# Performance work log

Hardware: AMD Instinct MI355X
Metric: run time of the kernel (lower is better)

Reference implementation:

```python
import jax, jax.numpy as jnp
import numpy as np

B, S, D, H = 4, 2048, 1024, 16
HD = D // H  # head dim = 64


def setup_inputs() -> dict:
    key = jax.random.key(0)
    ks = jax.random.split(key, 12)
    s = 1.0 / np.sqrt(D)
    return {
        "query": jax.random.normal(ks[0], (B, S, D), jnp.float32),
        "key": jax.random.normal(ks[1], (B, S, D), jnp.float32),
        "value": jax.random.normal(ks[2], (B, S, D), jnp.float32),
        "attention_mask": jnp.zeros((B, S, S), jnp.float32),
        "Wq": jax.random.normal(ks[3], (D, D), jnp.float32) * s,
        "bq": jax.random.normal(ks[4], (D,), jnp.float32) * s,
        "Wk": jax.random.normal(ks[5], (D, D), jnp.float32) * s,
        "bk": jax.random.normal(ks[6], (D,), jnp.float32) * s,
        "Wv": jax.random.normal(ks[7], (D, D), jnp.float32) * s,
        "bv": jax.random.normal(ks[8], (D,), jnp.float32) * s,
        "Wo": jax.random.normal(ks[9], (D, D), jnp.float32) * s,
        "bo": jax.random.normal(ks[10], (D,), jnp.float32) * s,
    }


def reference(query, key, value, attention_mask, Wq, bq, Wk, bk, Wv, bv, Wo, bo):
    # projections (torch Linear: x @ W.T + b)
    q = query @ Wq.T + bq
    k = key @ Wk.T + bk
    v = value @ Wv.T + bv
    # split heads: [B, S, D] -> [B, H, S, HD]
    split = lambda x: x.reshape(B, S, H, HD).transpose(0, 2, 1, 3)
    q, k, v = split(q), split(k), split(v)
    # scores: [B, H, Sq, Sk], scaled and masked (mask broadcast over heads)
    scores = jnp.einsum("bhqd,bhkd->bhqk", q, k) / jnp.sqrt(jnp.asarray(HD, q.dtype))
    scores = scores + attention_mask[:, None, :, :]
    probs = jax.nn.softmax(scores, axis=-1)
    out = jnp.einsum("bhqk,bhkd->bhqd", probs, v)
    # concat heads: [B, H, S, HD] -> [B, S, D]
    out = out.transpose(0, 2, 1, 3).reshape(B, S, D)
    return out @ Wo.T + bo
```

## Files before the change

### kernel.cpp

```cpp
#include <hip/hip_runtime.h>
#include <hip/hip_bf16.h>


typedef float f32x4 __attribute__((ext_vector_type(4)));
typedef float f32x16 __attribute__((ext_vector_type(16)));
typedef short bf16x8 __attribute__((ext_vector_type(8)));

#define LOG2E 1.4426950408889634f

__device__ __forceinline__ void gload_lds16(const void* g, void* l) {
  __builtin_amdgcn_global_load_lds((const __attribute__((address_space(1))) void*)g,
                                   (__attribute__((address_space(3))) void*)l,
                                   16, 0, 0);
}

__device__ __forceinline__ float fast_exp2(float x) {
#if __has_builtin(__builtin_amdgcn_exp2f)
  return __builtin_amdgcn_exp2f(x);
#else
  return exp2f(x);
#endif
}

__device__ __forceinline__ f32x16 vzero16() {
  f32x16 v;
#pragma unroll
  for (int i = 0; i < 16; i++) v[i] = 0.f;
  return v;
}

__device__ __forceinline__ unsigned bf16bits(float x) {
  __hip_bfloat16 h = __float2bfloat16(x);
  return (unsigned)*(unsigned short*)&h;
}

__device__ __forceinline__ void pl32swap(unsigned& a, unsigned& b, int hi) {
#if __has_builtin(__builtin_amdgcn_permlane32_swap)
  typedef unsigned uint2v __attribute__((ext_vector_type(2)));
  uint2v r = __builtin_amdgcn_permlane32_swap(a, b, false, false);
  a = r[0];
  b = r[1];
#else
  unsigned ax = __shfl_xor((int)a, 32);
  unsigned bx = __shfl_xor((int)b, 32);
  unsigned na = hi ? bx : a;
  unsigned nb = hi ? b : ax;
  a = na;
  b = nb;
#endif
}

__device__ __forceinline__ bf16x8 lds_read_swz(const __hip_bfloat16* base, int row, int colByte) {
  int off = row * 128 + (colByte ^ ((row & 7) << 4));
  return *(const bf16x8*)((const char*)base + off);
}

__global__ __launch_bounds__(256) void cvt3(const float* __restrict__ s0,
                                            const float* __restrict__ s1,
                                            const float* __restrict__ s2,
                                            __hip_bfloat16* __restrict__ d0,
                                            __hip_bfloat16* __restrict__ d1,
                                            __hip_bfloat16* __restrict__ d2, int n) {
  const float* s = blockIdx.z == 0 ? s0 : (blockIdx.z == 1 ? s1 : s2);
  __hip_bfloat16* d = blockIdx.z == 0 ? d0 : (blockIdx.z == 1 ? d1 : d2);
  int i = (blockIdx.x * 256 + threadIdx.x) * 8;
  if (i + 8 <= n) {
    float4 x = *(const float4*)(s + i);
    float4 y = *(const float4*)(s + i + 4);
    bf16x8 v;
    __hip_bfloat16* hv = (__hip_bfloat16*)&v;
    hv[0] = __float2bfloat16(x.x); hv[1] = __float2bfloat16(x.y);
    hv[2] = __float2bfloat16(x.z); hv[3] = __float2bfloat16(x.w);
    hv[4] = __float2bfloat16(y.x); hv[5] = __float2bfloat16(y.y);
    hv[6] = __float2bfloat16(y.z); hv[7] = __float2bfloat16(y.w);
    *(bf16x8*)(d + i) = v;
  }
}

__global__ __launch_bounds__(256) void cvt4(const float* __restrict__ s0,
                                            const float* __restrict__ s1,
                                            const float* __restrict__ s2,
                                            const float* __restrict__ s3,
                                            __hip_bfloat16* __restrict__ d0,
                                            __hip_bfloat16* __restrict__ d1,
                                            __hip_bfloat16* __restrict__ d2,
                                            __hip_bfloat16* __restrict__ d3, int n) {
  const float* s = blockIdx.z == 0 ? s0 : (blockIdx.z == 1 ? s1 : (blockIdx.z == 2 ? s2 : s3));
  __hip_bfloat16* d = blockIdx.z == 0 ? d0 : (blockIdx.z == 1 ? d1 : (blockIdx.z == 2 ? d2 : d3));
  int i = (blockIdx.x * 256 + threadIdx.x) * 8;
  if (i + 8 <= n) {
    float4 x = *(const float4*)(s + i);
    float4 y = *(const float4*)(s + i + 4);
    bf16x8 v;
    __hip_bfloat16* hv = (__hip_bfloat16*)&v;
    hv[0] = __float2bfloat16(x.x); hv[1] = __float2bfloat16(x.y);
    hv[2] = __float2bfloat16(x.z); hv[3] = __float2bfloat16(x.w);
    hv[4] = __float2bfloat16(y.x); hv[5] = __float2bfloat16(y.y);
    hv[6] = __float2bfloat16(y.z); hv[7] = __float2bfloat16(y.w);
    *(bf16x8*)(d + i) = v;
  }
}

template <int MODE>
__global__ __launch_bounds__(256) void gemm_nt(const __hip_bfloat16* __restrict__ A,
                                               const __hip_bfloat16* __restrict__ W,
                                               const float* __restrict__ bias,
                                               void* __restrict__ out) {
  extern __shared__ char smem[];
  __hip_bfloat16(*As)[64] = (__hip_bfloat16(*)[64])smem;
  __hip_bfloat16(*Bs)[64] = (__hip_bfloat16(*)[64])(smem + 128 * 64 * 2);

  const int t = threadIdx.x;
  const int w = t >> 6, l = t & 63;
  const int wm = w >> 1, wn = w & 1;
  const int rowbase = blockIdx.y * 128;
  const int colbase = blockIdx.x * 128;
  const int lr = l & 15, lg = l >> 4;
  const int srow = l >> 3, schunk = (l & 7) * 8;

  f32x4 acc[4][4];
#pragma unroll
  for (int m = 0; m < 4; m++)
#pragma unroll
    for (int n = 0; n < 4; n++) acc[m][n] = {0.f, 0.f, 0.f, 0.f};

  for (int kt = 0; kt < 16; ++kt) {
    const int k0 = kt * 64;
#pragma unroll
    for (int i = 0; i < 4; i++) {
      int r = w * 32 + i * 8;
      gload_lds16(A + (size_t)(rowbase + r + srow) * 1024 + k0 + schunk, &As[r][0]);
      gload_lds16(W + (size_t)(colbase + r + srow) * 1024 + k0 + schunk, &Bs[r][0]);
    }
    __syncthreads();
#pragma unroll
    for (int kk = 0; kk < 2; kk++) {
      bf16x8 a[4], b[4];
#pragma unroll
      for (int m = 0; m < 4; m++) a[m] = *(const bf16x8*)&As[wm * 64 + m * 16 + lr][kk * 32 + lg * 8];
#pragma unroll
      for (int n = 0; n < 4; n++) b[n] = *(const bf16x8*)&Bs[wn * 64 + n * 16 + lr][kk * 32 + lg * 8];
#pragma unroll
      for (int m = 0; m < 4; m++)
#pragma unroll
        for (int n = 0; n < 4; n++)
          acc[m][n] = __builtin_amdgcn_mfma_f32_16x16x32_bf16(a[m], b[n], acc[m][n], 0, 0, 0);
    }
    __syncthreads();
  }

  if (MODE == 0 || MODE == 2) {
#pragma unroll
    for (int m = 0; m < 4; m++) {
#pragma unroll
      for (int r = 0; r < 4; r++) {
        int gi = rowbase + wm * 64 + m * 16 + lg * 4 + r;
#pragma unroll
        for (int n = 0; n < 4; n++) {
          int gj = colbase + wn * 64 + n * 16 + lr;
          float v = acc[m][n][r] + bias[gj];
          if (MODE == 0)
            ((__hip_bfloat16*)out)[(size_t)gi * 1024 + gj] = __float2bfloat16(v);
          else
            ((float*)out)[(size_t)gi * 1024 + gj] = v;
        }
      }
    }
  } else {
    __hip_bfloat16* Ts = (__hip_bfloat16*)smem;
#pragma unroll
    for (int m = 0; m < 4; m++)
#pragma unroll
      for (int r = 0; r < 4; r++) {
        int rr = wm * 64 + m * 16 + lg * 4 + r;
#pragma unroll
        for (int n = 0; n < 4; n++) {
          int c = wn * 64 + n * 16 + lr;
          Ts[rr * 130 + c] = __float2bfloat16(acc[m][n][r] + bias[colbase + c]);
        }
      }
    __syncthreads();
    int d = t >> 1, s0 = (t & 1) * 64;
    int gd = colbase + d;
    int h = gd >> 6, hd = gd & 63;
    int gs = rowbase + s0;
    int b = gs >> 11, sl = gs & 2047;
    __hip_bfloat16* dst = (__hip_bfloat16*)out + ((size_t)(b * 16 + h) * 64 + hd) * 2048 + sl;
#pragma unroll
    for (int c8 = 0; c8 < 8; c8++) {
      bf16x8 v;
#pragma unroll
      for (int j = 0; j < 8; j++)
        ((unsigned short*)&v)[j] = ((const unsigned short*)Ts)[(s0 + c8 * 8 + j) * 130 + d];
      *(bf16x8*)(dst + c8 * 8) = v;
    }
  }
}

__global__ __launch_bounds__(256, 3) void attn(const __hip_bfloat16* __restrict__ Q,
                                               const __hip_bfloat16* __restrict__ K,
                                               const __hip_bfloat16* __restrict__ Vt,
                                               const float* __restrict__ mask,
                                               __hip_bfloat16* __restrict__ O) {
  __shared__ __hip_bfloat16 Ks[2][64][64];
  __shared__ __hip_bfloat16 Vs[2][64][64];

  const int t = threadIdx.x, w = t >> 6, l = t & 63;
  const int l31 = l & 31, hi = l >> 5;
  int lin = blockIdx.y * 16 + blockIdx.x;
  lin = (lin & 7) * 128 + (lin >> 3);
  const int qt = lin & 15, bh = lin >> 4;
  const int b = bh >> 4, h = bh & 15;
  const int q0 = qt * 128 + w * 32;
  const size_t bS = (size_t)b * 2048;
  const int srow = l >> 3;
  const int swchunk = ((l & 7) * 8) ^ (srow << 3);
  const float SCL = 0.125f * LOG2E;

#define STAGE(dbuf, ktile)                                                             \
  do {                                                                                 \
    int kb_ = (ktile) * 64;                                                            \
    _Pragma("unroll") for (int i_ = 0; i_ < 2; i_++) {                                 \
      int r_ = w * 16 + i_ * 8;                                                        \
      gload_lds16(K + (bS + kb_ + r_ + srow) * 1024 + h * 64 + swchunk,                \
                  &Ks[dbuf][r_][0]);                                                   \
      gload_lds16(Vt + ((size_t)bh * 64 + r_ + srow) * 2048 + kb_ + swchunk,           \
                  &Vs[dbuf][r_][0]);                                                   \
    }                                                                                  \
  } while (0)

  bf16x8 qf[4];
#pragma unroll
  for (int c = 0; c < 4; c++)
    qf[c] = *(const bf16x8*)(Q + (bS + q0 + l31) * 1024 + h * 64 + c * 16 + hi * 8);

  f32x16 acco[2];
  acco[0] = vzero16();
  acco[1] = vzero16();
  float m2 = -1e30f, lsum = 0.f;

  STAGE(0, 0);
  __syncthreads();
  int cur = 0;

  for (int kt = 0; kt < 32; ++kt) {
    const int kb = kt * 64;
    if (kt < 31) STAGE(cur ^ 1, kt + 1);

    float mvf[2][16];
#pragma unroll
    for (int ks = 0; ks < 2; ks++)
#pragma unroll
      for (int g = 0; g < 4; g++) {
        float4 tmp = *(const float4*)(mask + (bS + q0 + l31) * 2048 + kb + ks * 32 + g * 8 + hi * 4);
        mvf[ks][g * 4 + 0] = tmp.x; mvf[ks][g * 4 + 1] = tmp.y;
        mvf[ks][g * 4 + 2] = tmp.z; mvf[ks][g * 4 + 3] = tmp.w;
      }

    f32x16 sc[2];
    sc[0] = vzero16();
    sc[1] = vzero16();
    __builtin_amdgcn_s_setprio(1);
#pragma unroll
    for (int c = 0; c < 4; c++) {
      bf16x8 ka0 = lds_read_swz(&Ks[cur][0][0], l31, c * 32 + hi * 16);
      sc[0] = __builtin_amdgcn_mfma_f32_32x32x16_bf16(ka0, qf[c], sc[0], 0, 0, 0);
      bf16x8 ka1 = lds_read_swz(&Ks[cur][0][0], 32 + l31, c * 32 + hi * 16);
      sc[1] = __builtin_amdgcn_mfma_f32_32x32x16_bf16(ka1, qf[c], sc[1], 0, 0, 0);
    }
    __builtin_amdgcn_s_setprio(0);

    float s2[2][16];
#pragma unroll
    for (int ks = 0; ks < 2; ks++)
#pragma unroll
      for (int r = 0; r < 16; r++)
        s2[ks][r] = sc[ks][r] * SCL + mvf[ks][r] * LOG2E;

    float tmax = s2[0][0];
#pragma unroll
    for (int ks = 0; ks < 2; ks++)
#pragma unroll
      for (int r = 0; r < 16; r++) tmax = fmaxf(tmax, s2[ks][r]);
    tmax = fmaxf(tmax, __shfl_xor(tmax, 32));

    if (__any(tmax > m2 + 8.0f)) {
      float mn = fmaxf(m2, tmax);
      float rs = fast_exp2(m2 - mn);
      m2 = mn;
      lsum *= rs;
#pragma unroll
      for (int r = 0; r < 16; r++) {
        float rsr = __shfl(rs, (r & 3) + 8 * (r >> 2) + 4 * hi);
        acco[0][r] *= rsr;
        acco[1][r] *= rsr;
      }
    }

    float tsum = 0.f;
    unsigned pk[2][4][2];
#pragma unroll
    for (int ks = 0; ks < 2; ks++)
#pragma unroll
      for (int g = 0; g < 4; g++)
#pragma unroll
        for (int s = 0; s < 2; s++) {
          float p0 = fast_exp2(s2[ks][g * 4 + s * 2] - m2);
          float p1 = fast_exp2(s2[ks][g * 4 + s * 2 + 1] - m2);
          tsum += p0 + p1;
          pk[ks][g][s] = (bf16bits(p1) << 16) | bf16bits(p0);
        }
    tsum += __shfl_xor(tsum, 32);
    lsum += tsum;

    __builtin_amdgcn_s_setprio(1);
#pragma unroll
    for (int ks = 0; ks < 2; ks++) {
#pragma unroll
      for (int c16 = 0; c16 < 2; c16++) {
        unsigned x0 = pk[ks][2 * c16][0], y0 = pk[ks][2 * c16 + 1][0];
        unsigned x1 = pk[ks][2 * c16][1], y1 = pk[ks][2 * c16 + 1][1];
        pl32swap(x0, y0, hi);
        pl32swap(x1, y1, hi);
        bf16x8 pa;
        ((unsigned*)&pa)[0] = x0; ((unsigned*)&pa)[1] = x1;
        ((unsigned*)&pa)[2] = y0; ((unsigned*)&pa)[3] = y1;
#pragma unroll
        for (int ds = 0; ds < 2; ds++) {
          bf16x8 vb = lds_read_swz(&Vs[cur][0][0], ds * 32 + l31, ks * 64 + c16 * 32 + hi * 16);
          acco[ds] = __builtin_amdgcn_mfma_f32_32x32x16_bf16(pa, vb, acco[ds], 0, 0, 0);
        }
      }
    }
    __builtin_amdgcn_s_setprio(0);
    __syncthreads();
    cur ^= 1;
  }
#undef STAGE

  float inv = 1.0f / lsum;
#pragma unroll
  for (int r = 0; r < 16; r++) {
    float invr = __shfl(inv, (r & 3) + 8 * (r >> 2) + 4 * hi);
    int q = q0 + (r & 3) + 8 * (r >> 2) + 4 * hi;
#pragma unroll
    for (int ds = 0; ds < 2; ds++)
      O[(bS + q) * 1024 + h * 64 + ds * 32 + l31] = __float2bfloat16(acco[ds][r] * invr);
  }
}

extern "C" void kernel_launch(void* const* d_in, const int* in_sizes, int n_in,
                              void* d_out, int out_size, void* d_ws, size_t ws_size,
                              hipStream_t stream) {
  const float* q = (const float*)d_in[0];
  const float* k = (const float*)d_in[1];
  const float* v = (const float*)d_in[2];
  const float* msk = (const float*)d_in[3];
  const float* Wq = (const float*)d_in[4];
  const float* bq = (const float*)d_in[5];
  const float* Wk = (const float*)d_in[6];
  const float* bk = (const float*)d_in[7];
  const float* Wv = (const float*)d_in[8];
  const float* bv = (const float*)d_in[9];
  const float* Wo = (const float*)d_in[10];
  const float* bo = (const float*)d_in[11];

  char* ws = (char*)d_ws;
  __hip_bfloat16* qin = (__hip_bfloat16*)(ws);
  __hip_bfloat16* kin = (__hip_bfloat16*)(ws + (16u << 20));
  __hip_bfloat16* vin = (__hip_bfloat16*)(ws + (32u << 20));
  __hip_bfloat16* wqb = (__hip_bfloat16*)(ws + (48u << 20));
  __hip_bfloat16* wkb = (__hip_bfloat16*)(ws + (50u << 20));
  __hip_bfloat16* wvb = (__hip_bfloat16*)(ws + (52u << 20));
  __hip_bfloat16* wob = (__hip_bfloat16*)(ws + (54u << 20));
  __hip_bfloat16* vT  = (__hip_bfloat16*)(ws + (56u << 20));
  __hip_bfloat16* kp  = vin;
  __hip_bfloat16* qp  = kin;
  __hip_bfloat16* oat = qin;

  dim3 blk(256);
  size_t smem = 33280;

  cvt3<<<dim3(4096, 1, 3), blk, 0, stream>>>(q, k, v, qin, kin, vin, 8388608);
  cvt4<<<dim3(512, 1, 4), blk, 0, stream>>>(Wq, Wk, Wv, Wo, wqb, wkb, wvb, wob, 1048576);
  gemm_nt<1><<<dim3(8, 64), blk, smem, stream>>>(vin, wvb, bv, vT);
  gemm_nt<0><<<dim3(8, 64), blk, smem, stream>>>(kin, wkb, bk, kp);
  gemm_nt<0><<<dim3(8, 64), blk, smem, stream>>>(qin, wqb, bq, qp);
  attn<<<dim3(16, 64), blk, 0, stream>>>(qp, kp, vT, msk, oat);
  gemm_nt<2><<<dim3(8, 64), blk, smem, stream>>>(oat, wob, bo, (float*)d_out);
}
```

Before: 327.1 us.

## Fold softmax scale into Q projection and preload mask into MFMA accumulators

```diff
diff --git a/kernel.cpp b/kernel.cpp
--- a/kernel.cpp
+++ b/kernel.cpp
@@ -20,13 +20,6 @@
 #else
   return exp2f(x);
 #endif
-}
-
-__device__ __forceinline__ f32x16 vzero16() {
-  f32x16 v;
-#pragma unroll
-  for (int i = 0; i < 16; i++) v[i] = 0.f;
-  return v;
 }
 
 __device__ __forceinline__ unsigned bf16bits(float x) {
@@ -105,7 +98,7 @@
 __global__ __launch_bounds__(256) void gemm_nt(const __hip_bfloat16* __restrict__ A,
                                                const __hip_bfloat16* __restrict__ W,
                                                const float* __restrict__ bias,
-                                               void* __restrict__ out) {
+                                               void* __restrict__ out, float scale) {
   extern __shared__ char smem[];
   __hip_bfloat16(*As)[64] = (__hip_bfloat16(*)[64])smem;
   __hip_bfloat16(*Bs)[64] = (__hip_bfloat16(*)[64])(smem + 128 * 64 * 2);
@@ -158,7 +151,7 @@
 #pragma unroll
         for (int n = 0; n < 4; n++) {
           int gj = colbase + wn * 64 + n * 16 + lr;
-          float v = acc[m][n][r] + bias[gj];
+          float v = (acc[m][n][r] + bias[gj]) * scale;
           if (MODE == 0)
             ((__hip_bfloat16*)out)[(size_t)gi * 1024 + gj] = __float2bfloat16(v);
           else
@@ -197,7 +190,7 @@
   }
 }
 
-__global__ __launch_bounds__(256, 3) void attn(const __hip_bfloat16* __restrict__ Q,
+__global__ __launch_bounds__(256, 4) void attn(const __hip_bfloat16* __restrict__ Q,
                                                const __hip_bfloat16* __restrict__ K,
                                                const __hip_bfloat16* __restrict__ Vt,
                                                const float* __restrict__ mask,
@@ -215,7 +208,6 @@
   const size_t bS = (size_t)b * 2048;
   const int srow = l >> 3;
   const int swchunk = ((l & 7) * 8) ^ (srow << 3);
-  const float SCL = 0.125f * LOG2E;
 
 #define STAGE(dbuf, ktile)                                                             \
   do {                                                                                 \
@@ -235,31 +227,30 @@
     qf[c] = *(const bf16x8*)(Q + (bS + q0 + l31) * 1024 + h * 64 + c * 16 + hi * 8);
 
   f32x16 acco[2];
-  acco[0] = vzero16();
-  acco[1] = vzero16();
+#pragma unroll
+  for (int i = 0; i < 16; i++) { acco[0][i] = 0.f; acco[1][i] = 0.f; }
   float m2 = -1e30f, lsum = 0.f;
 
   STAGE(0, 0);
   __syncthreads();
   int cur = 0;
 
+  const float* mrow = mask + (bS + q0 + l31) * 2048;
+
   for (int kt = 0; kt < 32; ++kt) {
     const int kb = kt * 64;
     if (kt < 31) STAGE(cur ^ 1, kt + 1);
 
-    float mvf[2][16];
+    f32x16 sc[2];
 #pragma unroll
     for (int ks = 0; ks < 2; ks++)
 #pragma unroll
       for (int g = 0; g < 4; g++) {
-        float4 tmp = *(const float4*)(mask + (bS + q0 + l31) * 2048 + kb + ks * 32 + g * 8 + hi * 4);
-        mvf[ks][g * 4 + 0] = tmp.x; mvf[ks][g * 4 + 1] = tmp.y;
-        mvf[ks][g * 4 + 2] = tmp.z; mvf[ks][g * 4 + 3] = tmp.w;
-      }
-
-    f32x16 sc[2];
-    sc[0] = vzero16();
-    sc[1] = vzero16();
+        float4 tmp = *(const float4*)(mrow + kb + ks * 32 + g * 8 + hi * 4);
+        sc[ks][g * 4 + 0] = tmp.x * LOG2E; sc[ks][g * 4 + 1] = tmp.y * LOG2E;
+        sc[ks][g * 4 + 2] = tmp.z * LOG2E; sc[ks][g * 4 + 3] = tmp.w * LOG2E;
+      }
+
     __builtin_amdgcn_s_setprio(1);
 #pragma unroll
     for (int c = 0; c < 4; c++) {
@@ -270,19 +261,14 @@
     }
     __builtin_amdgcn_s_setprio(0);
 
-    float s2[2][16];
-#pragma unroll
-    for (int ks = 0; ks < 2; ks++)
-#pragma unroll
-      for (int r = 0; r < 16; r++)
-        s2[ks][r] = sc[ks][r] * SCL + mvf[ks][r] * LOG2E;
-
-    float tmax = s2[0][0];
-#pragma unroll
-    for (int ks = 0; ks < 2; ks++)
-#pragma unroll
-      for (int r = 0; r < 16; r++) tmax = fmaxf(tmax, s2[ks][r]);
-    tmax = fmaxf(tmax, __shfl_xor(tmax, 32));
+    float mx[16];
+#pragma unroll
+    for (int r = 0; r < 16; r++) mx[r] = fmaxf(sc[0][r], sc[1][r]);
+#pragma unroll
+    for (int s = 8; s >= 1; s >>= 1)
+#pragma unroll
+      for (int r = 0; r < s; r++) mx[r] = fmaxf(mx[r], mx[r + s]);
+    float tmax = fmaxf(mx[0], __shfl_xor(mx[0], 32));
 
     if (__any(tmax > m2 + 8.0f)) {
       float mn = fmaxf(m2, tmax);
@@ -297,7 +283,7 @@
       }
     }
 
-    float tsum = 0.f;
+    float ts0 = 0.f, ts1 = 0.f;
     unsigned pk[2][4][2];
 #pragma unroll
     for (int ks = 0; ks < 2; ks++)
@@ -305,11 +291,13 @@
       for (int g = 0; g < 4; g++)
 #pragma unroll
         for (int s = 0; s < 2; s++) {
-          float p0 = fast_exp2(s2[ks][g * 4 + s * 2] - m2);
-          float p1 = fast_exp2(s2[ks][g * 4 + s * 2 + 1] - m2);
-          tsum += p0 + p1;
+          float p0 = fast_exp2(sc[ks][g * 4 + s * 2] - m2);
+          float p1 = fast_exp2(sc[ks][g * 4 + s * 2 + 1] - m2);
+          ts0 += p0;
+          ts1 += p1;
           pk[ks][g][s] = (bf16bits(p1) << 16) | bf16bits(p0);
         }
+    float tsum = ts0 + ts1;
     tsum += __shfl_xor(tsum, 32);
     lsum += tsum;
 
@@ -380,12 +368,13 @@
 
   dim3 blk(256);
   size_t smem = 33280;
+  const float qscale = 0.125f * LOG2E;
 
   cvt3<<<dim3(4096, 1, 3), blk, 0, stream>>>(q, k, v, qin, kin, vin, 8388608);
   cvt4<<<dim3(512, 1, 4), blk, 0, stream>>>(Wq, Wk, Wv, Wo, wqb, wkb, wvb, wob, 1048576);
-  gemm_nt<1><<<dim3(8, 64), blk, smem, stream>>>(vin, wvb, bv, vT);
-  gemm_nt<0><<<dim3(8, 64), blk, smem, stream>>>(kin, wkb, bk, kp);
-  gemm_nt<0><<<dim3(8, 64), blk, smem, stream>>>(qin, wqb, bq, qp);
+  gemm_nt<1><<<dim3(8, 64), blk, smem, stream>>>(vin, wvb, bv, vT, 1.0f);
+  gemm_nt<0><<<dim3(8, 64), blk, smem, stream>>>(kin, wkb, bk, kp, 1.0f);
+  gemm_nt<0><<<dim3(8, 64), blk, smem, stream>>>(qin, wqb, bq, qp, qscale);
   attn<<<dim3(16, 64), blk, 0, stream>>>(qp, kp, vT, msk, oat);
-  gemm_nt<2><<<dim3(8, 64), blk, smem, stream>>>(oat, wob, bo, (float*)d_out);
-}
+  gemm_nt<2><<<dim3(8, 64), blk, smem, stream>>>(oat, wob, bo, (float*)d_out, 1.0f);
+}
```

New measurement: 313.8 us. -4.0%, faster.
